# Kernel tuning notes

Measured on AMD Instinct MI355X. Metric: run time of the kernel, lower is better.

## Reference

```python
import jax, jax.numpy as jnp
import numpy as np

B, S, C, H = 8, 1024, 512, 8
DH = C // H  # channels per head


def setup_inputs() -> dict:
    key = jax.random.key(0)
    ks = jax.random.split(key, 10)
    s = 1.0 / np.sqrt(C)
    return {
        "pe_lin_encoding": jax.random.normal(ks[0], (B, S, C), jnp.float32),
        "pe_lin_skip": jax.random.normal(ks[1], (B, S, C), jnp.float32),
        "Wq": jax.random.normal(ks[2], (C, C), jnp.float32) * s,
        "bq": jax.random.normal(ks[3], (C,), jnp.float32) * s,
        "Wk": jax.random.normal(ks[4], (C, C), jnp.float32) * s,
        "bk": jax.random.normal(ks[5], (C,), jnp.float32) * s,
        "Wv": jax.random.normal(ks[6], (C, C), jnp.float32) * s,
        "bv": jax.random.normal(ks[7], (C,), jnp.float32) * s,
        "Wo": jax.random.normal(ks[8], (C, C), jnp.float32) * s,
        "bo": jax.random.normal(ks[9], (C,), jnp.float32) * s,
    }


def reference(pe_lin_encoding, pe_lin_skip, Wq, bq, Wk, bk, Wv, bv, Wo, bo):
    # flatten trailing dims (already [B, S, C] here)
    x = pe_lin_encoding.reshape(pe_lin_encoding.shape[0], pe_lin_encoding.shape[1], -1)
    # torch Linear convention: y = x @ W^T + b, W is [out, in]
    q = jnp.einsum("bsc,oc->bso", x, Wq) + bq
    k = jnp.einsum("bsc,oc->bso", x, Wk) + bk
    v = jnp.einsum("bsc,oc->bso", x, Wv) + bv
    # split heads: [B, S, H, DH] -> attention per head
    q = q.reshape(B, S, H, DH)
    k = k.reshape(B, S, H, DH)
    v = v.reshape(B, S, H, DH)
    scale = 1.0 / np.sqrt(DH)
    scores = jnp.einsum("bqhd,bkhd->bhqk", q, k) * scale  # [B,H,S,S]
    attn = jax.nn.softmax(scores, axis=-1)
    ctx = jnp.einsum("bhqk,bkhd->bqhd", attn, v).reshape(B, S, C)
    out = jnp.einsum("bsc,oc->bso", ctx, Wo) + bo
    return out + pe_lin_skip
```

## Files before the change

### kernel.cpp

```cpp
#include <hip/hip_runtime.h>
#include <hip/hip_bf16.h>

typedef unsigned short u16;
typedef unsigned int u32;

constexpr int B  = 8;
constexpr int S  = 1024;
constexpr int C  = 512;
constexpr int H  = 8;
constexpr int DH = 64;
constexpr int M  = B * S;

typedef __attribute__((ext_vector_type(8))) short bf16x8;
typedef __attribute__((ext_vector_type(4))) float f32x4;

#define GLOBAL_AS __attribute__((address_space(1)))
#define LDS_AS    __attribute__((address_space(3)))

#define QSCALE 0.1803368867f

__device__ __forceinline__ float bf2f(u16 u) {
    return __uint_as_float(((u32)u) << 16);
}
__device__ __forceinline__ u16 f2bf(float f) {
    u32 u = __float_as_uint(f);
    u += 0x7fffu + ((u >> 16) & 1u);
    return (u16)(u >> 16);
}
__device__ __forceinline__ u32 pack2(float a, float b) {
    return (u32)f2bf(a) | ((u32)f2bf(b) << 16);
}
__device__ __forceinline__ void async_cp16(const u16* g, u16* l) {
    __builtin_amdgcn_global_load_lds((const GLOBAL_AS void*)g, (LDS_AS void*)l, 16, 0, 0);
}

constexpr int NX4 = M * C / 4;
constexpr int NW4 = C * C / 4;

__global__ __launch_bounds__(256) void cvt_kernel(
    const float* __restrict__ x,
    const float* __restrict__ wq, const float* __restrict__ wk,
    const float* __restrict__ wv, const float* __restrict__ wo,
    u16* __restrict__ xb, u16* __restrict__ wqkv, u16* __restrict__ wob)
{
    const int i = blockIdx.x * 256 + threadIdx.x;
    const float* src; u16* dst; int off;
    if      (i < NX4)          { src = x;  dst = xb;           off = i; }
    else if (i < NX4 +   NW4)  { src = wq; dst = wqkv;         off = i - NX4; }
    else if (i < NX4 + 2*NW4)  { src = wk; dst = wqkv + C*C;   off = i - NX4 -   NW4; }
    else if (i < NX4 + 3*NW4)  { src = wv; dst = wqkv + 2*C*C; off = i - NX4 - 2*NW4; }
    else                       { src = wo; dst = wob;          off = i - NX4 - 3*NW4; }
    float4 v = ((const float4*)src)[off];
    uint2 p; p.x = pack2(v.x, v.y); p.y = pack2(v.z, v.w);
    ((uint2*)dst)[off] = p;
}

__global__ __launch_bounds__(256) void qkv_gemm(
    const u16* __restrict__ xb, const u16* __restrict__ wqkv,
    const float* __restrict__ bq, const float* __restrict__ bk,
    const float* __restrict__ bv,
    u16* __restrict__ Qo, u16* __restrict__ Ko, u16* __restrict__ Vo)
{
    __shared__ alignas(16) u16 smem[128 * 136];
    u16* const Asm = smem;
    u16* const Bsm = smem + 128 * 64;

    const int mTile = blockIdx.x * 128;
    const int nTile = blockIdx.y * 128;
    const int t = threadIdx.x, lane = t & 63, w = t >> 6;
    const int ql = lane & 15, quad = lane >> 4;
    const int wm = (w & 1) * 64, wn = (w >> 1) * 64;

    f32x4 acc[4][4];
    #pragma unroll
    for (int i = 0; i < 4; i++)
        #pragma unroll
        for (int j = 0; j < 4; j++) acc[i][j] = (f32x4){0.f, 0.f, 0.f, 0.f};

    for (int k0 = 0; k0 < C; k0 += 64) {
        __syncthreads();
        #pragma unroll
        for (int q = 0; q < 4; q++) {
            const int chunk = q * 256 + t;
            const int row = chunk >> 3, c8 = (chunk & 7) * 8;
            async_cp16(xb   + (size_t)(mTile + row) * C + k0 + c8, &Asm[row * 64 + c8]);
            async_cp16(wqkv + (size_t)(nTile + row) * C + k0 + c8, &Bsm[row * 64 + c8]);
        }
        __syncthreads();

        #pragma unroll
        for (int ks = 0; ks < 64; ks += 32) {
            bf16x8 af[4], bfr[4];
            #pragma unroll
            for (int i = 0; i < 4; i++)
                af[i] = *(const bf16x8*)&Asm[(wm + i*16 + ql) * 64 + ks + quad*8];
            #pragma unroll
            for (int j = 0; j < 4; j++)
                bfr[j] = *(const bf16x8*)&Bsm[(wn + j*16 + ql) * 64 + ks + quad*8];
            #pragma unroll
            for (int i = 0; i < 4; i++)
                #pragma unroll
                for (int j = 0; j < 4; j++)
                    acc[i][j] = __builtin_amdgcn_mfma_f32_16x16x32_bf16(af[i], bfr[j], acc[i][j], 0, 0, 0);
        }
    }

    const int z = nTile >> 9;
    const int nBase = nTile & 511;
    if (z == 2) {
        __syncthreads();
        u16* const T = smem;
        #pragma unroll
        for (int j = 0; j < 4; j++) {
            const int n = wn + j*16 + ql;
            const float bj = bv[nBase + n];
            #pragma unroll
            for (int i = 0; i < 4; i++)
                #pragma unroll
                for (int r = 0; r < 4; r++)
                    T[n * 136 + wm + i*16 + quad*4 + r] = f2bf(acc[i][j][r] + bj);
        }
        __syncthreads();
        const int bb = mTile >> 10, ssBase = mTile & 1023;
        #pragma unroll
        for (int q = 0; q < 8; q++) {
            const int c = q * 256 + t;
            const int row = c >> 4, col = (c & 15) * 8;
            const int o = nBase + row, h = o >> 6, d = o & 63;
            *(float4*)(Vo + ((size_t)((bb*H + h) * DH + d)) * S + ssBase + col) =
                *(const float4*)&T[row * 136 + col];
        }
    } else {
        const float* bias = (z == 0) ? bq : bk;
        u16* dst          = (z == 0) ? Qo : Ko;
        const float sc    = (z == 0) ? QSCALE : 1.0f;
        #pragma unroll
        for (int j = 0; j < 4; j++) {
            const int o = nBase + wn + j*16 + ql;
            const float bj = bias[o];
            const int h = o >> 6, d = o & 63;
            #pragma unroll
            for (int i = 0; i < 4; i++) {
                #pragma unroll
                for (int r = 0; r < 4; r++) {
                    const int m = mTile + wm + i*16 + quad*4 + r;
                    const int bb = m >> 10, ss = m & 1023;
                    dst[(size_t)((bb*H + h) * S + ss) * DH + d] = f2bf((acc[i][j][r] + bj) * sc);
                }
            }
        }
    }
}

__global__ __launch_bounds__(256) void attn_kernel(
    const u16* __restrict__ Qo,
    const u16* __restrict__ Ko,
    const u16* __restrict__ Vo,
    u16* __restrict__ ctx)
{
    __shared__ alignas(16) u16 KsU[64 * 64];
    __shared__ alignas(16) u16 VsU[64 * 64];
    __shared__ alignas(16) u16 Ps [64 * 72];

    const int g = blockIdx.x;
    const int xcd = g & 7, slot = g >> 3;
    const int bh = xcd * 8 + (slot >> 4);
    const int qt = slot & 15;

    const int t = threadIdx.x;
    const int lane = t & 63, w = t >> 6;
    const int ql = lane & 15, quad = lane >> 4;

    const u16* Qb = Qo + (size_t)bh * S * DH;
    const u16* Kb = Ko + (size_t)bh * S * DH;
    const u16* Vt = Vo + (size_t)bh * DH * S;

    const int qrow = qt*64 + w*16 + ql;
    const bf16x8 qf0 = *(const bf16x8*)(Qb + (size_t)qrow * DH + quad*8);
    const bf16x8 qf1 = *(const bf16x8*)(Qb + (size_t)qrow * DH + 32 + quad*8);

    bf16x8 onesf;
    #pragma unroll
    for (int i = 0; i < 8; i++) onesf[i] = (short)0x3F80;

    const int swzA = ((quad       ^ (ql & 7)) << 3);
    const int swzB = (((quad + 4) ^ (ql & 7)) << 3);

    f32x4 acc[4], accl;
    #pragma unroll
    for (int dt = 0; dt < 4; dt++) acc[dt] = (f32x4){0.f, 0.f, 0.f, 0.f};
    accl = (f32x4){0.f, 0.f, 0.f, 0.f};

    for (int k0 = 0; k0 < S; k0 += 64) {
        __syncthreads();
        #pragma unroll
        for (int q = 0; q < 2; q++) {
            const int idx = q * 256 + t;
            const int row = idx >> 3, cc = idx & 7;
            const int scol = ((cc ^ (row & 7)) << 3);
            float4 kv = *(const float4*)(Kb + (size_t)(k0 + row) * DH + cc*8);
            float4 vv = *(const float4*)(Vt + (size_t)row * S + k0 + cc*8);
            *(float4*)&KsU[row * 64 + scol] = kv;
            *(float4*)&VsU[row * 64 + scol] = vv;
        }
        __syncthreads();

        f32x4 sc[4];
        #pragma unroll
        for (int nt = 0; nt < 4; nt++) {
            sc[nt] = (f32x4){0.f, 0.f, 0.f, 0.f};
            const bf16x8 kf0 = *(const bf16x8*)&KsU[(nt*16 + ql) * 64 + swzA];
            const bf16x8 kf1 = *(const bf16x8*)&KsU[(nt*16 + ql) * 64 + swzB];
            sc[nt] = __builtin_amdgcn_mfma_f32_16x16x32_bf16(qf0, kf0, sc[nt], 0, 0, 0);
            sc[nt] = __builtin_amdgcn_mfma_f32_16x16x32_bf16(qf1, kf1, sc[nt], 0, 0, 0);
        }

        #pragma unroll
        for (int r = 0; r < 4; r++) {
            const int prow = w*16 + quad*4 + r;
            Ps[prow * 72 +  0 + ql] = f2bf(exp2f(sc[0][r]));
            Ps[prow * 72 + 16 + ql] = f2bf(exp2f(sc[1][r]));
            Ps[prow * 72 + 32 + ql] = f2bf(exp2f(sc[2][r]));
            Ps[prow * 72 + 48 + ql] = f2bf(exp2f(sc[3][r]));
        }

        #pragma unroll
        for (int c = 0; c < 2; c++) {
            const bf16x8 pf = *(const bf16x8*)&Ps[(w*16 + ql) * 72 + c*32 + quad*8];
            const int swz = (c == 0) ? swzA : swzB;
            #pragma unroll
            for (int dt = 0; dt < 4; dt++) {
                const bf16x8 vf = *(const bf16x8*)&VsU[(dt*16 + ql) * 64 + swz];
                acc[dt] = __builtin_amdgcn_mfma_f32_16x16x32_bf16(pf, vf, acc[dt], 0, 0, 0);
            }
            accl = __builtin_amdgcn_mfma_f32_16x16x32_bf16(pf, onesf, accl, 0, 0, 0);
        }
    }

    const int b_ = bh >> 3, h = bh & 7;
    #pragma unroll
    for (int r = 0; r < 4; r++) {
        const float inv = 1.0f / accl[r];
        const int srow = qt*64 + w*16 + quad*4 + r;
        const size_t base = ((size_t)(b_*S + srow)) * C + h*DH;
        #pragma unroll
        for (int dt = 0; dt < 4; dt++)
            ctx[base + dt*16 + ql] = f2bf(acc[dt][r] * inv);
    }
}

__global__ __launch_bounds__(256) void out_gemm(
    const u16* __restrict__ ctx, const u16* __restrict__ wob,
    const float* __restrict__ bo, const float* __restrict__ skip,
    float* __restrict__ out)
{
    __shared__ alignas(16) u16 Asm[128 * 64];
    __shared__ alignas(16) u16 Bsm[128 * 64];

    const int mTile = blockIdx.x * 128;
    const int nTile = blockIdx.y * 128;
    const int t = threadIdx.x, lane = t & 63, w = t >> 6;
    const int ql = lane & 15, quad = lane >> 4;
    const int wm = (w & 1) * 64, wn = (w >> 1) * 64;

    f32x4 acc[4][4];
    #pragma unroll
    for (int i = 0; i < 4; i++)
        #pragma unroll
        for (int j = 0; j < 4; j++) acc[i][j] = (f32x4){0.f, 0.f, 0.f, 0.f};

    for (int k0 = 0; k0 < C; k0 += 64) {
        __syncthreads();
        #pragma unroll
        for (int q = 0; q < 4; q++) {
            const int chunk = q * 256 + t;
            const int row = chunk >> 3, c8 = (chunk & 7) * 8;
            async_cp16(ctx + (size_t)(mTile + row) * C + k0 + c8, &Asm[row * 64 + c8]);
            async_cp16(wob + (size_t)(nTile + row) * C + k0 + c8, &Bsm[row * 64 + c8]);
        }
        __syncthreads();

        #pragma unroll
        for (int ks = 0; ks < 64; ks += 32) {
            bf16x8 af[4], bfr[4];
            #pragma unroll
            for (int i = 0; i < 4; i++)
                af[i] = *(const bf16x8*)&Asm[(wm + i*16 + ql) * 64 + ks + quad*8];
            #pragma unroll
            for (int j = 0; j < 4; j++)
                bfr[j] = *(const bf16x8*)&Bsm[(wn + j*16 + ql) * 64 + ks + quad*8];
            #pragma unroll
            for (int i = 0; i < 4; i++)
                #pragma unroll
                for (int j = 0; j < 4; j++)
                    acc[i][j] = __builtin_amdgcn_mfma_f32_16x16x32_bf16(af[i], bfr[j], acc[i][j], 0, 0, 0);
        }
    }

    #pragma unroll
    for (int j = 0; j < 4; j++) {
        const int o = nTile + wn + j*16 + ql;
        const float bj = bo[o];
        #pragma unroll
        for (int i = 0; i < 4; i++) {
            #pragma unroll
            for (int r = 0; r < 4; r++) {
                const int m = mTile + wm + i*16 + quad*4 + r;
                const size_t idx = (size_t)m * C + o;
                out[idx] = acc[i][j][r] + bj + skip[idx];
            }
        }
    }
}

extern "C" void kernel_launch(void* const* d_in, const int* in_sizes, int n_in,
                              void* d_out, int out_size, void* d_ws, size_t ws_size,
                              hipStream_t stream) {
    (void)in_sizes; (void)n_in; (void)out_size; (void)ws_size;
    const float* x    = (const float*)d_in[0];
    const float* skip = (const float*)d_in[1];
    const float* Wq   = (const float*)d_in[2];
    const float* bq   = (const float*)d_in[3];
    const float* Wk   = (const float*)d_in[4];
    const float* bk   = (const float*)d_in[5];
    const float* Wv   = (const float*)d_in[6];
    const float* bv   = (const float*)d_in[7];
    const float* Wo   = (const float*)d_in[8];
    const float* bo   = (const float*)d_in[9];
    float* out = (float*)d_out;

    u16* xb   = (u16*)d_ws;
    u16* wqkv = xb   + (size_t)M * C;
    u16* wob  = wqkv + (size_t)3 * C * C;
    u16* Qo   = wob  + (size_t)C * C;
    u16* Ko   = Qo   + (size_t)B * H * S * DH;
    u16* Vo   = Ko   + (size_t)B * H * S * DH;
    u16* ctx  = xb;

    cvt_kernel<<<dim3((NX4 + 4 * NW4) / 256), 256, 0, stream>>>(
        x, Wq, Wk, Wv, Wo, xb, wqkv, wob);
    qkv_gemm<<<dim3(M / 128, 1536 / 128), 256, 0, stream>>>(
        xb, wqkv, bq, bk, bv, Qo, Ko, Vo);
    attn_kernel<<<dim3(1024), 256, 0, stream>>>(Qo, Ko, Vo, ctx);
    out_gemm<<<dim3(M / 128, C / 128), 256, 0, stream>>>(
        ctx, wob, bo, skip, out);
}
```

Before: 175.7 us.

## Stage Q/K GEMM epilogue through LDS and store row-major for coalesced writes

The Q and K outputs of the QKV GEMM now go through the shared-memory transpose buffer, as V already did, and are written as 16-byte vectors in a row-major [B*S, C] layout instead of scattered 2-byte stores into a per-head layout. The attention kernel's Q and K reads are changed to use a row stride of C with a per-head column offset. This is meant to cut the cost of uncoalesced global stores in the GEMM epilogue. In exchange it adds an LDS round trip and barriers on the Q/K path, and the attention K loads become strided 128-byte row segments.

```diff
diff --git a/kernel.cpp b/kernel.cpp
--- a/kernel.cpp
+++ b/kernel.cpp
@@ -107,20 +107,29 @@
 
     const int z = nTile >> 9;
     const int nBase = nTile & 511;
+    const float* bias = (z == 0) ? bq : (z == 1) ? bk : bv;
+    const float sc    = (z == 0) ? QSCALE : 1.0f;
+
+    __syncthreads();
+    u16* const T = smem;
+    #pragma unroll
+    for (int j = 0; j < 4; j++) {
+        const int n = wn + j*16 + ql;
+        const float bj = bias[nBase + n];
+        #pragma unroll
+        for (int i = 0; i < 4; i++) {
+            #pragma unroll
+            for (int r = 0; r < 4; r++) {
+                const int m = wm + i*16 + quad*4 + r;
+                const u16 val = f2bf((acc[i][j][r] + bj) * sc);
+                if (z == 2) T[n * 136 + m] = val;
+                else        T[m * 136 + n] = val;
+            }
+        }
+    }
+    __syncthreads();
+
     if (z == 2) {
-        __syncthreads();
-        u16* const T = smem;
-        #pragma unroll
-        for (int j = 0; j < 4; j++) {
-            const int n = wn + j*16 + ql;
-            const float bj = bv[nBase + n];
-            #pragma unroll
-            for (int i = 0; i < 4; i++)
-                #pragma unroll
-                for (int r = 0; r < 4; r++)
-                    T[n * 136 + wm + i*16 + quad*4 + r] = f2bf(acc[i][j][r] + bj);
-        }
-        __syncthreads();
         const int bb = mTile >> 10, ssBase = mTile & 1023;
         #pragma unroll
         for (int q = 0; q < 8; q++) {
@@ -131,23 +140,13 @@
                 *(const float4*)&T[row * 136 + col];
         }
     } else {
-        const float* bias = (z == 0) ? bq : bk;
-        u16* dst          = (z == 0) ? Qo : Ko;
-        const float sc    = (z == 0) ? QSCALE : 1.0f;
-        #pragma unroll
-        for (int j = 0; j < 4; j++) {
-            const int o = nBase + wn + j*16 + ql;
-            const float bj = bias[o];
-            const int h = o >> 6, d = o & 63;
-            #pragma unroll
-            for (int i = 0; i < 4; i++) {
-                #pragma unroll
-                for (int r = 0; r < 4; r++) {
-                    const int m = mTile + wm + i*16 + quad*4 + r;
-                    const int bb = m >> 10, ss = m & 1023;
-                    dst[(size_t)((bb*H + h) * S + ss) * DH + d] = f2bf((acc[i][j][r] + bj) * sc);
-                }
-            }
+        u16* dst = (z == 0) ? Qo : Ko;
+        #pragma unroll
+        for (int q = 0; q < 8; q++) {
+            const int c = q * 256 + t;
+            const int row = c >> 4, col = (c & 15) * 8;
+            *(float4*)(dst + (size_t)(mTile + row) * C + nBase + col) =
+                *(const float4*)&T[row * 136 + col];
         }
     }
 }
@@ -166,18 +165,19 @@
     const int xcd = g & 7, slot = g >> 3;
     const int bh = xcd * 8 + (slot >> 4);
     const int qt = slot & 15;
+    const int b_ = bh >> 3, h = bh & 7;
 
     const int t = threadIdx.x;
     const int lane = t & 63, w = t >> 6;
     const int ql = lane & 15, quad = lane >> 4;
 
-    const u16* Qb = Qo + (size_t)bh * S * DH;
-    const u16* Kb = Ko + (size_t)bh * S * DH;
+    const u16* Qb = Qo + (size_t)b_ * S * C + h * DH;
+    const u16* Kb = Ko + (size_t)b_ * S * C + h * DH;
     const u16* Vt = Vo + (size_t)bh * DH * S;
 
     const int qrow = qt*64 + w*16 + ql;
-    const bf16x8 qf0 = *(const bf16x8*)(Qb + (size_t)qrow * DH + quad*8);
-    const bf16x8 qf1 = *(const bf16x8*)(Qb + (size_t)qrow * DH + 32 + quad*8);
+    const bf16x8 qf0 = *(const bf16x8*)(Qb + (size_t)qrow * C + quad*8);
+    const bf16x8 qf1 = *(const bf16x8*)(Qb + (size_t)qrow * C + 32 + quad*8);
 
     bf16x8 onesf;
     #pragma unroll
@@ -198,7 +198,7 @@
             const int idx = q * 256 + t;
             const int row = idx >> 3, cc = idx & 7;
             const int scol = ((cc ^ (row & 7)) << 3);
-            float4 kv = *(const float4*)(Kb + (size_t)(k0 + row) * DH + cc*8);
+            float4 kv = *(const float4*)(Kb + (size_t)(k0 + row) * C + cc*8);
             float4 vv = *(const float4*)(Vt + (size_t)row * S + k0 + cc*8);
             *(float4*)&KsU[row * 64 + scol] = kv;
             *(float4*)&VsU[row * 64 + scol] = vv;
@@ -237,7 +237,6 @@
         }
     }
 
-    const int b_ = bh >> 3, h = bh & 7;
     #pragma unroll
     for (int r = 0; r < 4; r++) {
         const float inv = 1.0f / accl[r];
@@ -333,8 +332,8 @@
     u16* wqkv = xb   + (size_t)M * C;
     u16* wob  = wqkv + (size_t)3 * C * C;
     u16* Qo   = wob  + (size_t)C * C;
-    u16* Ko   = Qo   + (size_t)B * H * S * DH;
-    u16* Vo   = Ko   + (size_t)B * H * S * DH;
+    u16* Ko   = Qo   + (size_t)M * C;
+    u16* Vo   = Ko   + (size_t)M * C;
     u16* ctx  = xb;
 
     cvt_kernel<<<dim3((NX4 + 4 * NW4) / 256), 256, 0, stream>>>(
```

New measurement: 180.2 us. 2.6% more time.
